# Optimization experiments

Measured on AMD Instinct MI355X. Metric: run time of the kernel, lower is better.

The kernel has to match this reference:

```python
import jax, jax.numpy as jnp
import numpy as np

B, IN, OUT, LUT_SIZE = 32, 8192, 16384, 256


def setup_inputs() -> dict:
    key = jax.random.key(0)
    k1, k2, k3 = jax.random.split(key, 3)
    x = jax.random.normal(k1, (B, IN), dtype=jnp.float32)
    # int8 weight codes, stored as indices in [0, 256) into the dequant LUT
    weight_idx = jax.random.randint(k2, (OUT, IN), 0, LUT_SIZE, dtype=jnp.int32)
    # symmetric uniform dequant levels: code c -> (c - 128) * scale
    scale = jnp.float32(0.05 / 128.0)
    lut = (jnp.arange(LUT_SIZE, dtype=jnp.float32) - 128.0) * scale  # [256]
    bias = jax.random.normal(k3, (OUT,), dtype=jnp.float32) * 0.02
    return {"x": x, "lut": lut, "bias": bias, "weight_idx": weight_idx}


def reference(x, lut, bias, weight_idx):
    # LUT dequantization: gather fp32 weight values from the 256-entry table
    W = lut[weight_idx]                      # [OUT, IN] fp32
    # y = x @ W^T + b   (einsum: b=batch tokens, i=in_features, o=out_features)
    return jnp.einsum("bi,oi->bo", x, W) + bias  # [B, OUT]
```

## Files before the change

### kernel.cpp

```cpp
#include <hip/hip_runtime.h>

#define IN_F   8192
#define OUT_F  16384
#define BATCH  32
#define KT     512
#define NTILES (IN_F / KT)
#define PITCH  2064

typedef __attribute__((ext_vector_type(8))) short  bf16x8;
typedef __attribute__((ext_vector_type(4))) float  f32x4;

__device__ __forceinline__ unsigned f2bf(float f) {
    unsigned u = __builtin_bit_cast(unsigned, f);
    return (u + 0x7fffu + ((u >> 16) & 1u)) >> 16;
}

__device__ __forceinline__ unsigned pk_i2bf(int a, int b) {
    unsigned fa = __builtin_bit_cast(unsigned, (float)a);
    unsigned fb = __builtin_bit_cast(unsigned, (float)b);
#if __has_builtin(__builtin_amdgcn_perm)
    return __builtin_amdgcn_perm(fb, fa, 0x07060302u);
#else
    return (fa >> 16) | (fb & 0xffff0000u);
#endif
}

__device__ __forceinline__ void async_copy16(const int* g, void* l) {
    __builtin_amdgcn_global_load_lds(
        (const __attribute__((address_space(1))) unsigned*)g,
        (__attribute__((address_space(3))) unsigned*)l,
        16, 0, 0);
}

__global__ __launch_bounds__(256) void prep_kernel(
        const float* __restrict__ x, const float* __restrict__ lut,
        unsigned short* __restrict__ xbf, float* __restrict__ sumx) {
    const int b = blockIdx.x;
    const int t = threadIdx.x;
    const float s = lut[129];
    const float4* xr = (const float4*)(x + b * IN_F);
    ushort4* xo = (ushort4*)(xbf + b * IN_F);
    float acc = 0.f;
    #pragma unroll
    for (int i = 0; i < IN_F / 4 / 256; ++i) {
        float4 v = xr[t + i * 256];
        acc += v.x + v.y + v.z + v.w;
        ushort4 o;
        o.x = (unsigned short)f2bf(v.x * s);
        o.y = (unsigned short)f2bf(v.y * s);
        o.z = (unsigned short)f2bf(v.z * s);
        o.w = (unsigned short)f2bf(v.w * s);
        xo[t + i * 256] = o;
    }
    __shared__ float red[256];
    red[t] = acc;
    __syncthreads();
    for (int off = 128; off > 0; off >>= 1) {
        if (t < off) red[t] += red[t + off];
        __syncthreads();
    }
    if (t == 0) sumx[b] = red[0];
}

__global__ __launch_bounds__(256, 4) void gemm_kernel(
        const unsigned short* __restrict__ xbf,
        const int* __restrict__ widx,
        const float* __restrict__ bias,
        const float* __restrict__ lut,
        const float* __restrict__ sumx,
        float* __restrict__ out) {
    __shared__ char ltile[16 * PITCH];
    const int tid   = threadIdx.x;
    const int wave  = tid >> 6;
    const int lane  = tid & 63;
    const int col16 = lane & 15;
    const int quad  = lane >> 4;
    const int n0    = blockIdx.x * 16;

    const unsigned short* xp0 = xbf + col16 * IN_F + quad * 8;
    const unsigned short* xp1 = xp0 + 16 * IN_F;

    f32x4 acc0 = {0.f, 0.f, 0.f, 0.f};
    f32x4 acc1 = {0.f, 0.f, 0.f, 0.f};

    for (int t = 0; t < NTILES; ++t) {
        const long kt = (long)t * KT;
        #pragma unroll
        for (int j = 0; j < 8; ++j) {
            const int r = wave * 4 + (j >> 1);
            const int h = j & 1;
            async_copy16(widx + (long)(n0 + r) * IN_F + kt + h * 256 + lane * 4,
                         ltile + r * PITCH + h * 1024);
        }
        asm volatile("s_waitcnt vmcnt(0)" ::: "memory");
        __syncthreads();
        #pragma unroll
        for (int s = 0; s < 4; ++s) {
            const char* bb = ltile + col16 * PITCH + wave * 512 + s * 128 + quad * 32;
            int4 c0 = *(const int4*)(bb);
            int4 c1 = *(const int4*)(bb + 16);
            const long ka = kt + wave * 128 + s * 32;
            bf16x8 a0 = *(const bf16x8*)(xp0 + ka);
            bf16x8 a1 = *(const bf16x8*)(xp1 + ka);
            union { unsigned u[4]; bf16x8 v; } bB;
            bB.u[0] = pk_i2bf(c0.x, c0.y);
            bB.u[1] = pk_i2bf(c0.z, c0.w);
            bB.u[2] = pk_i2bf(c1.x, c1.y);
            bB.u[3] = pk_i2bf(c1.z, c1.w);
            acc0 = __builtin_amdgcn_mfma_f32_16x16x32_bf16(a0, bB.v, acc0, 0, 0, 0);
            acc1 = __builtin_amdgcn_mfma_f32_16x16x32_bf16(a1, bB.v, acc1, 0, 0, 0);
        }
        __syncthreads();
    }

    float* red = (float*)ltile;
    #pragma unroll
    for (int r = 0; r < 4; ++r) {
        red[wave * 512 + (quad * 4 + r)      * 16 + col16] = acc0[r];
        red[wave * 512 + (quad * 4 + r + 16) * 16 + col16] = acc1[r];
    }
    __syncthreads();
    const float l0 = lut[0];
    #pragma unroll
    for (int e0 = 0; e0 < 2; ++e0) {
        const int e = tid + e0 * 256;
        float v = red[e] + red[e + 512] + red[e + 1024] + red[e + 1536];
        const int m  = e >> 4;
        const int nn = e & 15;
        v += bias[n0 + nn] + l0 * sumx[m];
        out[(long)m * OUT_F + n0 + nn] = v;
    }
}

extern "C" void kernel_launch(void* const* d_in, const int* in_sizes, int n_in,
                              void* d_out, int out_size, void* d_ws, size_t ws_size,
                              hipStream_t stream) {
    const float* x    = (const float*)d_in[0];
    const float* lut  = (const float*)d_in[1];
    const float* bias = (const float*)d_in[2];
    const int*   widx = (const int*)d_in[3];
    float* out = (float*)d_out;

    unsigned short* xbf = (unsigned short*)d_ws;
    float* sumx = (float*)((char*)d_ws + BATCH * IN_F * 2);

    prep_kernel<<<BATCH, 256, 0, stream>>>(x, lut, xbf, sumx);
    gemm_kernel<<<OUT_F / 16, 256, 0, stream>>>(xbf, widx, bias, lut, sumx, out);
}
```

Baseline: 700.2 us.

## Repack int32 weight codes to tiled bytes and double-buffer GEMM LDS tiles

Adds a pack kernel that narrows each int32 weight code to a byte and lays the codes out in contiguous per-block, per-K-tile slabs. The GEMM then streams these 1-byte codes into double-buffered LDS tiles with KT doubled, prefetching the next tile while computing the current one, and decodes bytes to bf16 in registers. The aim is to cut GEMM weight traffic by a factor of four and hide load latency. In exchange, the repack runs on every call and reads the full int32 array plus writes a new buffer, so total memory traffic goes up. It also needs a large workspace.

```diff
diff --git a/kernel.cpp b/kernel.cpp
--- a/kernel.cpp
+++ b/kernel.cpp
@@ -3,9 +3,9 @@
 #define IN_F   8192
 #define OUT_F  16384
 #define BATCH  32
-#define KT     512
-#define NTILES (IN_F / KT)
-#define PITCH  2064
+#define KT     1024
+#define NT     (IN_F / KT)
+#define PITCH  1040
 
 typedef __attribute__((ext_vector_type(8))) short  bf16x8;
 typedef __attribute__((ext_vector_type(4))) float  f32x4;
@@ -15,17 +15,17 @@
     return (u + 0x7fffu + ((u >> 16) & 1u)) >> 16;
 }
 
-__device__ __forceinline__ unsigned pk_i2bf(int a, int b) {
-    unsigned fa = __builtin_bit_cast(unsigned, (float)a);
-    unsigned fb = __builtin_bit_cast(unsigned, (float)b);
+__device__ __forceinline__ unsigned pk_ff(float fa, float fb) {
+    unsigned ua = __builtin_bit_cast(unsigned, fa);
+    unsigned ub = __builtin_bit_cast(unsigned, fb);
 #if __has_builtin(__builtin_amdgcn_perm)
-    return __builtin_amdgcn_perm(fb, fa, 0x07060302u);
+    return __builtin_amdgcn_perm(ub, ua, 0x07060302u);
 #else
-    return (fa >> 16) | (fb & 0xffff0000u);
+    return (ua >> 16) | (ub & 0xffff0000u);
 #endif
 }
 
-__device__ __forceinline__ void async_copy16(const int* g, void* l) {
+__device__ __forceinline__ void async_copy16(const void* g, void* l) {
     __builtin_amdgcn_global_load_lds(
         (const __attribute__((address_space(1))) unsigned*)g,
         (__attribute__((address_space(3))) unsigned*)l,
@@ -62,14 +62,36 @@
     if (t == 0) sumx[b] = red[0];
 }
 
+__global__ __launch_bounds__(256) void pack_kernel(
+        const int* __restrict__ widx, unsigned char* __restrict__ wpk) {
+    const long g  = (long)blockIdx.x * 256 + threadIdx.x;
+    const long i0 = g * 16;
+    const int  n  = (int)(i0 >> 13);
+    const int  k  = (int)(i0 & 8191);
+    const int  b  = n >> 4;
+    const int  r  = n & 15;
+    const int  t  = k >> 10;
+    const int  k0 = k & 1023;
+    const int4* src = (const int4*)(widx + i0);
+    unsigned tmp[4];
+    #pragma unroll
+    for (int q = 0; q < 4; ++q) {
+        int4 c = src[q];
+        tmp[q] = (c.x & 255) | ((c.y & 255) << 8) |
+                 ((c.z & 255) << 16) | ((unsigned)(c.w & 255) << 24);
+    }
+    uint4 o = {tmp[0], tmp[1], tmp[2], tmp[3]};
+    *(uint4*)(wpk + (((long)(b * NT + t) * 16 + r) << 10) + k0) = o;
+}
+
 __global__ __launch_bounds__(256, 4) void gemm_kernel(
         const unsigned short* __restrict__ xbf,
-        const int* __restrict__ widx,
+        const unsigned char* __restrict__ wpk,
         const float* __restrict__ bias,
         const float* __restrict__ lut,
         const float* __restrict__ sumx,
         float* __restrict__ out) {
-    __shared__ char ltile[16 * PITCH];
+    __shared__ char ltile[2][16 * PITCH];
     const int tid   = threadIdx.x;
     const int wave  = tid >> 6;
     const int lane  = tid & 63;
@@ -77,40 +99,51 @@
     const int quad  = lane >> 4;
     const int n0    = blockIdx.x * 16;
 
+    const unsigned char* slab = wpk + ((long)blockIdx.x * NT) * (16 * KT);
     const unsigned short* xp0 = xbf + col16 * IN_F + quad * 8;
     const unsigned short* xp1 = xp0 + 16 * IN_F;
 
     f32x4 acc0 = {0.f, 0.f, 0.f, 0.f};
     f32x4 acc1 = {0.f, 0.f, 0.f, 0.f};
 
-    for (int t = 0; t < NTILES; ++t) {
-        const long kt = (long)t * KT;
+    #define STAGE(tt, bb)                                                     \
+        _Pragma("unroll")                                                     \
+        for (int j = 0; j < 4; ++j) {                                         \
+            const int r_ = wave * 4 + j;                                      \
+            async_copy16(slab + ((long)(tt) * 16 + r_) * KT + lane * 16,      \
+                         &ltile[bb][r_ * PITCH]);                             \
+        }
+
+    STAGE(0, 0)
+    for (int t = 0; t < NT; ++t) {
+        if (t < NT - 1) {
+            STAGE(t + 1, (t + 1) & 1)
+            asm volatile("s_waitcnt vmcnt(4)" ::: "memory");
+        } else {
+            asm volatile("s_waitcnt vmcnt(0)" ::: "memory");
+        }
+        asm volatile("s_barrier" ::: "memory");
+        const char* base = &ltile[t & 1][col16 * PITCH + wave * 256 + quad * 8];
         #pragma unroll
-        for (int j = 0; j < 8; ++j) {
-            const int r = wave * 4 + (j >> 1);
-            const int h = j & 1;
-            async_copy16(widx + (long)(n0 + r) * IN_F + kt + h * 256 + lane * 4,
-                         ltile + r * PITCH + h * 1024);
-        }
-        asm volatile("s_waitcnt vmcnt(0)" ::: "memory");
-        __syncthreads();
-        #pragma unroll
-        for (int s = 0; s < 4; ++s) {
-            const char* bb = ltile + col16 * PITCH + wave * 512 + s * 128 + quad * 32;
-            int4 c0 = *(const int4*)(bb);
-            int4 c1 = *(const int4*)(bb + 16);
-            const long ka = kt + wave * 128 + s * 32;
+        for (int s = 0; s < 8; ++s) {
+            unsigned p0 = *(const unsigned*)(base + s * 32);
+            unsigned p1 = *(const unsigned*)(base + s * 32 + 4);
+            const int ka = t * KT + wave * 256 + s * 32;
             bf16x8 a0 = *(const bf16x8*)(xp0 + ka);
             bf16x8 a1 = *(const bf16x8*)(xp1 + ka);
+            float f0 = (float)(p0 & 255u),         f1 = (float)((p0 >> 8) & 255u);
+            float f2 = (float)((p0 >> 16) & 255u), f3 = (float)(p0 >> 24);
+            float f4 = (float)(p1 & 255u),         f5 = (float)((p1 >> 8) & 255u);
+            float f6 = (float)((p1 >> 16) & 255u), f7 = (float)(p1 >> 24);
             union { unsigned u[4]; bf16x8 v; } bB;
-            bB.u[0] = pk_i2bf(c0.x, c0.y);
-            bB.u[1] = pk_i2bf(c0.z, c0.w);
-            bB.u[2] = pk_i2bf(c1.x, c1.y);
-            bB.u[3] = pk_i2bf(c1.z, c1.w);
+            bB.u[0] = pk_ff(f0, f1);
+            bB.u[1] = pk_ff(f2, f3);
+            bB.u[2] = pk_ff(f4, f5);
+            bB.u[3] = pk_ff(f6, f7);
             acc0 = __builtin_amdgcn_mfma_f32_16x16x32_bf16(a0, bB.v, acc0, 0, 0, 0);
             acc1 = __builtin_amdgcn_mfma_f32_16x16x32_bf16(a1, bB.v, acc1, 0, 0, 0);
         }
-        __syncthreads();
+        asm volatile("s_barrier" ::: "memory");
     }
 
     float* red = (float*)ltile;
@@ -143,7 +176,9 @@
 
     unsigned short* xbf = (unsigned short*)d_ws;
     float* sumx = (float*)((char*)d_ws + BATCH * IN_F * 2);
+    unsigned char* wpk = (unsigned char*)d_ws + (1 << 20);
 
     prep_kernel<<<BATCH, 256, 0, stream>>>(x, lut, xbf, sumx);
-    gemm_kernel<<<OUT_F / 16, 256, 0, stream>>>(xbf, widx, bias, lut, sumx, out);
+    pack_kernel<<<(long)OUT_F * IN_F / 16 / 256, 256, 0, stream>>>(widx, wpk);
+    gemm_kernel<<<OUT_F / 16, 256, 0, stream>>>(xbf, wpk, bias, lut, sumx, out);
 }
```

New measurement: 765.6 us. +9.4%, slower.

## Double-buffer LDS weight tiles and prefetch activations ahead of MFMA compute

Applied to the files above, without the earlier changes.

Halves the K tile to 256 and keeps two LDS buffers, so the async global-to-LDS load of the next weight tile and the register prefetch of the next activation fragments are in flight while the current tile is being computed. The single vmcnt(0) wait plus syncthreads per tile becomes a partial vmcnt wait and raw s_barrier calls. The aim is to hide global memory latency in this bandwidth-bound int32-weight GEMM. The cost is more register use for the prefetched activations, more barriers, and correctness that depends on the hand-counted vmcnt values.

```diff
diff --git a/kernel.cpp b/kernel.cpp
--- a/kernel.cpp
+++ b/kernel.cpp
@@ -3,9 +3,9 @@
 #define IN_F   8192
 #define OUT_F  16384
 #define BATCH  32
-#define KT     512
-#define NTILES (IN_F / KT)
-#define PITCH  2064
+#define KT     256
+#define NT     (IN_F / KT)
+#define PITCH  1040
 
 typedef __attribute__((ext_vector_type(8))) short  bf16x8;
 typedef __attribute__((ext_vector_type(4))) float  f32x4;
@@ -25,7 +25,7 @@
 #endif
 }
 
-__device__ __forceinline__ void async_copy16(const int* g, void* l) {
+__device__ __forceinline__ void async_copy16(const void* g, void* l) {
     __builtin_amdgcn_global_load_lds(
         (const __attribute__((address_space(1))) unsigned*)g,
         (__attribute__((address_space(3))) unsigned*)l,
@@ -69,7 +69,7 @@
         const float* __restrict__ lut,
         const float* __restrict__ sumx,
         float* __restrict__ out) {
-    __shared__ char ltile[16 * PITCH];
+    __shared__ char ltile[2][16 * PITCH];
     const int tid   = threadIdx.x;
     const int wave  = tid >> 6;
     const int lane  = tid & 63;
@@ -77,40 +77,74 @@
     const int quad  = lane >> 4;
     const int n0    = blockIdx.x * 16;
 
+    const int* slab = widx + (long)n0 * IN_F;
     const unsigned short* xp0 = xbf + col16 * IN_F + quad * 8;
     const unsigned short* xp1 = xp0 + 16 * IN_F;
 
     f32x4 acc0 = {0.f, 0.f, 0.f, 0.f};
     f32x4 acc1 = {0.f, 0.f, 0.f, 0.f};
 
-    for (int t = 0; t < NTILES; ++t) {
-        const long kt = (long)t * KT;
-        #pragma unroll
-        for (int j = 0; j < 8; ++j) {
-            const int r = wave * 4 + (j >> 1);
-            const int h = j & 1;
-            async_copy16(widx + (long)(n0 + r) * IN_F + kt + h * 256 + lane * 4,
-                         ltile + r * PITCH + h * 1024);
+    #define STAGE(tt, bb)                                                     \
+        _Pragma("unroll")                                                     \
+        for (int j_ = 0; j_ < 4; ++j_) {                                      \
+            const int r_ = wave * 4 + j_;                                     \
+            async_copy16(slab + (long)r_ * IN_F + (tt) * KT + lane * 4,       \
+                         &ltile[bb][r_ * PITCH]);                             \
         }
-        asm volatile("s_waitcnt vmcnt(0)" ::: "memory");
-        __syncthreads();
-        #pragma unroll
-        for (int s = 0; s < 4; ++s) {
-            const char* bb = ltile + col16 * PITCH + wave * 512 + s * 128 + quad * 32;
-            int4 c0 = *(const int4*)(bb);
-            int4 c1 = *(const int4*)(bb + 16);
-            const long ka = kt + wave * 128 + s * 32;
-            bf16x8 a0 = *(const bf16x8*)(xp0 + ka);
-            bf16x8 a1 = *(const bf16x8*)(xp1 + ka);
-            union { unsigned u[4]; bf16x8 v; } bB;
-            bB.u[0] = pk_i2bf(c0.x, c0.y);
-            bB.u[1] = pk_i2bf(c0.z, c0.w);
-            bB.u[2] = pk_i2bf(c1.x, c1.y);
-            bB.u[3] = pk_i2bf(c1.z, c1.w);
-            acc0 = __builtin_amdgcn_mfma_f32_16x16x32_bf16(a0, bB.v, acc0, 0, 0, 0);
-            acc1 = __builtin_amdgcn_mfma_f32_16x16x32_bf16(a1, bB.v, acc1, 0, 0, 0);
+
+    #define ALOAD(dst, tt)                                                    \
+        do {                                                                  \
+            const int ka_ = (tt) * KT + wave * 64;                            \
+            dst[0] = *(const bf16x8*)(xp0 + ka_);                             \
+            dst[1] = *(const bf16x8*)(xp1 + ka_);                             \
+            dst[2] = *(const bf16x8*)(xp0 + ka_ + 32);                        \
+            dst[3] = *(const bf16x8*)(xp1 + ka_ + 32);                        \
+        } while (0)
+
+    #define COMPUTE(tt, bb, ar)                                               \
+        _Pragma("unroll")                                                     \
+        for (int s_ = 0; s_ < 2; ++s_) {                                      \
+            const char* b_ = &ltile[bb][col16 * PITCH + wave * 256            \
+                                        + s_ * 128 + quad * 32];              \
+            int4 c0 = *(const int4*)(b_);                                     \
+            int4 c1 = *(const int4*)(b_ + 16);                                \
+            union { unsigned u[4]; bf16x8 v; } bB;                            \
+            bB.u[0] = pk_i2bf(c0.x, c0.y);                                    \
+            bB.u[1] = pk_i2bf(c0.z, c0.w);                                    \
+            bB.u[2] = pk_i2bf(c1.x, c1.y);                                    \
+            bB.u[3] = pk_i2bf(c1.z, c1.w);                                    \
+            acc0 = __builtin_amdgcn_mfma_f32_16x16x32_bf16(                   \
+                       ar[s_ * 2],     bB.v, acc0, 0, 0, 0);                  \
+            acc1 = __builtin_amdgcn_mfma_f32_16x16x32_bf16(                   \
+                       ar[s_ * 2 + 1], bB.v, acc1, 0, 0, 0);                  \
         }
-        __syncthreads();
+
+    bf16x8 aE[4], aO[4];
+    STAGE(0, 0)
+    ALOAD(aE, 0);
+
+    #pragma unroll
+    for (int t = 0; t < NT; t += 2) {
+        if (t + 1 < NT) {
+            STAGE(t + 1, 1)
+            ALOAD(aO, t + 1);
+            asm volatile("s_waitcnt vmcnt(8)" ::: "memory");
+        } else {
+            asm volatile("s_waitcnt vmcnt(0)" ::: "memory");
+        }
+        __builtin_amdgcn_s_barrier();
+        COMPUTE(t, 0, aE)
+        __builtin_amdgcn_s_barrier();
+        if (t + 2 < NT) {
+            STAGE(t + 2, 0)
+            ALOAD(aE, t + 2);
+            asm volatile("s_waitcnt vmcnt(8)" ::: "memory");
+        } else {
+            asm volatile("s_waitcnt vmcnt(0)" ::: "memory");
+        }
+        __builtin_amdgcn_s_barrier();
+        COMPUTE(t + 1, 1, aO)
+        __builtin_amdgcn_s_barrier();
     }
 
     float* red = (float*)ltile;
```

Measured after the change: 683.9 us. 1.02x faster.
